# Performance work log

Measured on AMD Instinct MI355X. Metric: run time of the kernel, lower is better.

Reference implementation:

```python
import jax, jax.numpy as jnp
import numpy as np

B, S, D, H = 4, 2048, 1024, 16
DH = D // H  # 64


def setup_inputs() -> dict:
    key = jax.random.key(0)
    ks = jax.random.split(key, 11)
    s = 0.02
    return {
        "query": jax.random.normal(ks[0], (B, S, D), jnp.float32),
        "key": jax.random.normal(ks[1], (B, S, D), jnp.float32),
        "value": jax.random.normal(ks[2], (B, S, D), jnp.float32),
        "Wq": jax.random.normal(ks[3], (D, D), jnp.float32) * s,
        "bq": jnp.zeros((D,), jnp.float32),
        "Wk": jax.random.normal(ks[4], (D, D), jnp.float32) * s,
        "bk": jnp.zeros((D,), jnp.float32),
        "Wv": jax.random.normal(ks[5], (D, D), jnp.float32) * s,
        "bv": jnp.zeros((D,), jnp.float32),
        "Wo": jax.random.normal(ks[6], (D, D), jnp.float32) * s,
        "bo": jnp.zeros((D,), jnp.float32),
    }


def reference(query, key, value, Wq, bq, Wk, bk, Wv, bv, Wo, bo):
    b, s, _ = query.shape
    # linear projections (torch Linear: x @ W^T + b; here W stored as [in, out])
    q = query @ Wq + bq
    k = key @ Wk + bk
    v = value @ Wv + bv
    # split heads -> [B, H, S, DH]
    q = q.reshape(b, s, H, DH).transpose(0, 2, 1, 3)
    k = k.reshape(b, s, H, DH).transpose(0, 2, 1, 3)
    v = v.reshape(b, s, H, DH).transpose(0, 2, 1, 3)
    scale = jnp.sqrt(jnp.asarray(DH, jnp.float32))
    attn = jnp.einsum("bhqd,bhkd->bhqk", q, k) / scale  # [B,H,S,S]
    attn = jax.nn.softmax(attn, axis=-1)
    out = jnp.einsum("bhqk,bhkd->bhqd", attn, v)
    out = out.transpose(0, 2, 1, 3).reshape(b, s, D)
    return out @ Wo + bo
```

## Files before the change

kernel.cpp:

```cpp
#include <hip/hip_runtime.h>

typedef float f32x4 __attribute__((ext_vector_type(4)));
typedef __bf16 bf16x8 __attribute__((ext_vector_type(8)));
typedef unsigned short u16;
typedef unsigned int u32;
typedef u16 u16x4 __attribute__((ext_vector_type(4)));
typedef u16 u16x8 __attribute__((ext_vector_type(8)));
typedef u32 u32x2 __attribute__((ext_vector_type(2)));
typedef u32 u32x4 __attribute__((ext_vector_type(4)));

constexpr int Bn = 4, Sn = 2048, Dn = 1024, Hn = 16, DHn = 64;
constexpr int Mn = Bn * Sn;

static __device__ __forceinline__ u16 f2bf(float f) {
  return __builtin_bit_cast(u16, (__bf16)f);
}

static __device__ __forceinline__ u32 cvtpk(float lo, float hi) {
  u32 r;
  asm("v_cvt_pk_bf16_f32 %0, %1, %2" : "=v"(r) : "v"(lo), "v"(hi));
  return r;
}

static __device__ __forceinline__ void async16(const void* g, void* l) {
  __builtin_amdgcn_global_load_lds((const __attribute__((address_space(1))) u32*)g,
                                   (__attribute__((address_space(3))) u32*)l, 16, 0, 0);
}

static __device__ __forceinline__ void wait_bar2() {
  asm volatile("s_waitcnt vmcnt(2)" ::: "memory");
  __builtin_amdgcn_sched_barrier(0);
  __builtin_amdgcn_s_barrier();
  __builtin_amdgcn_sched_barrier(0);
}
static __device__ __forceinline__ void wait_bar8() {
  asm volatile("s_waitcnt vmcnt(8)" ::: "memory");
  __builtin_amdgcn_sched_barrier(0);
  __builtin_amdgcn_s_barrier();
  __builtin_amdgcn_sched_barrier(0);
}
static __device__ __forceinline__ void wait_bar0() {
  asm volatile("s_waitcnt vmcnt(0)" ::: "memory");
  __builtin_amdgcn_sched_barrier(0);
  __builtin_amdgcn_s_barrier();
  __builtin_amdgcn_sched_barrier(0);
}
static __device__ __forceinline__ void raw_bar() {
  __builtin_amdgcn_sched_barrier(0);
  __builtin_amdgcn_s_barrier();
  __builtin_amdgcn_sched_barrier(0);
}

__global__ void __launch_bounds__(256) cvt3_kernel(const float* __restrict__ q,
                                                   const float* __restrict__ k,
                                                   const float* __restrict__ v,
                                                   u16* __restrict__ dst) {
  const int i = blockIdx.x * 256 + threadIdx.x;
  const int t = i >> 20;
  const int li = i & 1048575;
  const float* s = (t == 0) ? q : (t == 1) ? k : v;
  const f32x4* sp = (const f32x4*)s + (size_t)li * 2;
  const f32x4 a = sp[0], b = sp[1];
  u16x8 o;
  o[0] = f2bf(a[0]); o[1] = f2bf(a[1]); o[2] = f2bf(a[2]); o[3] = f2bf(a[3]);
  o[4] = f2bf(b[0]); o[5] = f2bf(b[1]); o[6] = f2bf(b[2]); o[7] = f2bf(b[3]);
  ((u16x8*)dst)[i] = o;
}

__global__ void __launch_bounds__(256) transpose4_kernel(const float* __restrict__ Wq,
                                                         const float* __restrict__ Wk,
                                                         const float* __restrict__ Wv,
                                                         const float* __restrict__ Wo,
                                                         u16* __restrict__ Wts) {
  __shared__ float tile[32][33];
  const int z = blockIdx.z;
  const float* W = (z == 0) ? Wq : (z == 1) ? Wk : (z == 2) ? Wv : Wo;
  u16* Wt = Wts + (size_t)z * Dn * Dn;
  const int n0 = blockIdx.x * 32, k0 = blockIdx.y * 32;
  const int tx = threadIdx.x & 31, ty = (threadIdx.x >> 5) * 4;
#pragma unroll
  for (int i = 0; i < 4; ++i)
    tile[ty + i][tx] = W[(size_t)(k0 + ty + i) * Dn + n0 + tx];
  __syncthreads();
#pragma unroll
  for (int i = 0; i < 4; ++i)
    Wt[(size_t)(n0 + ty + i) * Dn + k0 + tx] = f2bf(tile[tx][ty + i]);
}

__global__ void __launch_bounds__(256) gemm_qkv_kernel(const u16* __restrict__ X,
                                                       const u16* __restrict__ Wts,
                                                       const float* __restrict__ bq,
                                                       const float* __restrict__ bk,
                                                       const float* __restrict__ bv,
                                                       u16* __restrict__ outbase) {
  __shared__ u16 As[2][128 * 64];
  __shared__ u16 Bs[2][128 * 64];

  const int bid = blockIdx.x;
  const int xcd = bid & 7;
  const int loc = bid >> 3;
  const int nb = loc & 7;
  const int panel = xcd * 24 + (loc >> 3);
  const int z = panel >> 6;
  const int m0 = (panel & 63) * 128, n0 = nb * 128;

  const u16* A = X + (size_t)z * Mn * Dn;
  const u16* Bt = Wts + (size_t)z * Dn * Dn;
  const float* bias = (z == 0) ? bq : (z == 1) ? bk : bv;
  u16* outp = outbase + (size_t)z * Mn * Dn;
  const float scale = (z == 0) ? 0.125f * 1.4426950408889634f : 1.0f;

  const int tid = threadIdx.x;
  const int wave = tid >> 6, lane = tid & 63;
  const int g = lane >> 4, c = lane & 15;
  const int wm = wave >> 1, wn = wave & 1;
  const int srow = lane >> 3, blk = lane & 7;

  f32x4 acc[4][4] = {};
  constexpr int NK = Dn / 64;

#pragma unroll
  for (int p = 0; p < 2; ++p) {
    const int k0 = p * 64;
#pragma unroll
    for (int i = 0; i < 4; ++i) {
      const int ch = wave * 4 + i;
      const int row = ch * 8 + srow;
      const int sblk = blk ^ srow;
      async16(A + (size_t)(m0 + row) * Dn + k0 + sblk * 8, As[p] + ch * 512);
      async16(Bt + (size_t)(n0 + row) * Dn + k0 + sblk * 8, Bs[p] + ch * 512);
    }
  }

  for (int k = 0; k < NK; ++k) {
    const int cur = k & 1;
    if (k + 1 < NK) wait_bar8(); else wait_bar0();

#pragma unroll
    for (int kk = 0; kk < 2; ++kk) {
      bf16x8 af[4], bfr[4];
#pragma unroll
      for (int mi = 0; mi < 4; ++mi)
        af[mi] = *(const bf16x8*)(As[cur] + (wm * 64 + mi * 16 + c) * 64 +
                                  (((kk * 4 + g) ^ (c & 7)) * 8));
#pragma unroll
      for (int ni = 0; ni < 4; ++ni)
        bfr[ni] = *(const bf16x8*)(Bs[cur] + (wn * 64 + ni * 16 + c) * 64 +
                                   (((kk * 4 + g) ^ (c & 7)) * 8));
#pragma unroll
      for (int mi = 0; mi < 4; ++mi)
#pragma unroll
        for (int ni = 0; ni < 4; ++ni)
          acc[mi][ni] = __builtin_amdgcn_mfma_f32_16x16x32_bf16(af[mi], bfr[ni],
                                                                acc[mi][ni], 0, 0, 0);
    }

    raw_bar();
    if (k + 2 < NK) {
      const int k0 = (k + 2) * 64;
#pragma unroll
      for (int i = 0; i < 4; ++i) {
        const int ch = wave * 4 + i;
        const int row = ch * 8 + srow;
        const int sblk = blk ^ srow;
        async16(A + (size_t)(m0 + row) * Dn + k0 + sblk * 8, As[cur] + ch * 512);
        async16(Bt + (size_t)(n0 + row) * Dn + k0 + sblk * 8, Bs[cur] + ch * 512);
      }
    }
  }

  const bool vmode = (z == 2);
#pragma unroll
  for (int ni = 0; ni < 4; ++ni) {
    const int col = n0 + wn * 64 + ni * 16 + c;
    const float bv = bias[col];
    const int hh = col >> 6, dh = col & 63;
#pragma unroll
    for (int mi = 0; mi < 4; ++mi) {
      const int row = m0 + wm * 64 + mi * 16 + g * 4;
      const int bb = row >> 11, s = row & 2047;
      if (!vmode) {
        u16* o = outp + (((size_t)(bb * Hn + hh) * Sn + s) * DHn + dh);
#pragma unroll
        for (int r = 0; r < 4; ++r)
          o[(size_t)r * DHn] = f2bf((acc[mi][ni][r] + bv) * scale);
      } else {
        u16x4 pk;
#pragma unroll
        for (int r = 0; r < 4; ++r) pk[r] = f2bf(acc[mi][ni][r] + bv);
        *(u16x4*)(outp + ((size_t)(bb * Hn + hh) * DHn + dh) * Sn + s) = pk;
      }
    }
  }
}

__global__ void __launch_bounds__(256) gemm_o_kernel(const u16* __restrict__ A,
                                                     const u16* __restrict__ Bt,
                                                     const float* __restrict__ bias,
                                                     float* __restrict__ outp) {
  __shared__ u16 As[2][128 * 64];
  __shared__ u16 Bs[2][128 * 64];
  const int bid = blockIdx.x;
  const int xcd = bid & 7;
  const int loc = bid >> 3;
  const int nb = loc & 7;
  const int panel = xcd * 8 + (loc >> 3);
  const int m0 = panel * 128, n0 = nb * 128;

  const int tid = threadIdx.x;
  const int wave = tid >> 6, lane = tid & 63;
  const int g = lane >> 4, c = lane & 15;
  const int wm = wave >> 1, wn = wave & 1;
  const int srow = lane >> 3, blk = lane & 7;

  f32x4 acc[4][4] = {};
  constexpr int NK = Dn / 64;

#pragma unroll
  for (int p = 0; p < 2; ++p) {
    const int k0 = p * 64;
#pragma unroll
    for (int i = 0; i < 4; ++i) {
      const int ch = wave * 4 + i;
      const int row = ch * 8 + srow;
      const int sblk = blk ^ srow;
      async16(A + (size_t)(m0 + row) * Dn + k0 + sblk * 8, As[p] + ch * 512);
      async16(Bt + (size_t)(n0 + row) * Dn + k0 + sblk * 8, Bs[p] + ch * 512);
    }
  }

  for (int k = 0; k < NK; ++k) {
    const int cur = k & 1;
    if (k + 1 < NK) wait_bar8(); else wait_bar0();

#pragma unroll
    for (int kk = 0; kk < 2; ++kk) {
      bf16x8 af[4], bfr[4];
#pragma unroll
      for (int mi = 0; mi < 4; ++mi)
        af[mi] = *(const bf16x8*)(As[cur] + (wm * 64 + mi * 16 + c) * 64 +
                                  (((kk * 4 + g) ^ (c & 7)) * 8));
#pragma unroll
      for (int ni = 0; ni < 4; ++ni)
        bfr[ni] = *(const bf16x8*)(Bs[cur] + (wn * 64 + ni * 16 + c) * 64 +
                                   (((kk * 4 + g) ^ (c & 7)) * 8));
#pragma unroll
      for (int mi = 0; mi < 4; ++mi)
#pragma unroll
        for (int ni = 0; ni < 4; ++ni)
          acc[mi][ni] = __builtin_amdgcn_mfma_f32_16x16x32_bf16(af[mi], bfr[ni],
                                                                acc[mi][ni], 0, 0, 0);
    }

    raw_bar();
    if (k + 2 < NK) {
      const int k0 = (k + 2) * 64;
#pragma unroll
      for (int i = 0; i < 4; ++i) {
        const int ch = wave * 4 + i;
        const int row = ch * 8 + srow;
        const int sblk = blk ^ srow;
        async16(A + (size_t)(m0 + row) * Dn + k0 + sblk * 8, As[cur] + ch * 512);
        async16(Bt + (size_t)(n0 + row) * Dn + k0 + sblk * 8, Bs[cur] + ch * 512);
      }
    }
  }

#pragma unroll
  for (int ni = 0; ni < 4; ++ni) {
    const int col = n0 + wn * 64 + ni * 16 + c;
    const float bv = bias[col];
#pragma unroll
    for (int mi = 0; mi < 4; ++mi) {
      const int row = m0 + wm * 64 + mi * 16 + g * 4;
      float* o = outp + (size_t)row * Dn + col;
#pragma unroll
      for (int r = 0; r < 4; ++r) o[(size_t)r * Dn] = acc[mi][ni][r] + bv;
    }
  }
}

__global__ void __launch_bounds__(512, 4) attn_kernel(const u16* __restrict__ Q,
                                                      const u16* __restrict__ Kp,
                                                      const u16* __restrict__ VT,
                                                      u16* __restrict__ O) {
  __shared__ u16 Ks[3][64 * 64];
  __shared__ u16 Vs[3][64 * 64];
  const int tid = threadIdx.x;
  const int wave = tid >> 6, lane = tid & 63;
  const int g = lane >> 4, c = lane & 15;
  const int bh = blockIdx.x;
  const int q0 = blockIdx.y * 256 + wave * 32;
  const u16* Qb = Q + (size_t)bh * Sn * DHn;
  const u16* Kb = Kp + (size_t)bh * Sn * DHn;
  const u16* Vb = VT + (size_t)bh * DHn * Sn;

  bf16x8 qf[2][2];
#pragma unroll
  for (int fq = 0; fq < 2; ++fq)
#pragma unroll
    for (int kk = 0; kk < 2; ++kk)
      qf[fq][kk] = *(const bf16x8*)(Qb + (size_t)(q0 + fq * 16 + c) * DHn + kk * 32 + g * 8);

  f32x4 ot[4][2] = {};
  f32x4 lacc[2] = {};
  u16x8 one8u;
#pragma unroll
  for (int j = 0; j < 8; ++j) one8u[j] = 0x3F80;
  const bf16x8 one8 = __builtin_bit_cast(bf16x8, one8u);
  const f32x4 zf = {};

  const int srow = lane >> 3, blk = lane & 7;
  const int krow = wave * 8 + srow;
  const int sblk = blk ^ srow;
  constexpr int NT = Sn / 64;

  u16 *kA = Ks[0], *kB = Ks[1], *kC = Ks[2];
  u16 *vA = Vs[0], *vB = Vs[1], *vC = Vs[2];

#pragma unroll
  for (int tt = 0; tt < 2; ++tt) {
    const int kt = tt * 64;
    async16(Kb + (size_t)(kt + krow) * DHn + sblk * 8, Ks[tt] + wave * 512);
    async16(Vb + (size_t)krow * Sn + kt + sblk * 8, Vs[tt] + wave * 512);
  }

  for (int t = 0; t < NT; ++t) {
    if (t + 1 < NT) wait_bar2(); else wait_bar0();

    if (t + 2 < NT) {
      const int kt = (t + 2) * 64;
      async16(Kb + (size_t)(kt + krow) * DHn + sblk * 8, kC + wave * 512);
      async16(Vb + (size_t)krow * Sn + kt + sblk * 8, vC + wave * 512);
    }

    f32x4 st[4][2];
    {
      bf16x8 kf[4];
#pragma unroll
      for (int fk = 0; fk < 4; ++fk)
        kf[fk] = *(const bf16x8*)(kA + (fk * 16 + c) * 64 + ((g ^ (c & 7)) * 8));
      __builtin_amdgcn_s_setprio(1);
#pragma unroll
      for (int fk = 0; fk < 4; ++fk)
#pragma unroll
        for (int fq = 0; fq < 2; ++fq)
          st[fk][fq] = __builtin_amdgcn_mfma_f32_16x16x32_bf16(kf[fk], qf[fq][0],
                                                               zf, 0, 0, 0);
      __builtin_amdgcn_s_setprio(0);
#pragma unroll
      for (int fk = 0; fk < 4; ++fk)
        kf[fk] = *(const bf16x8*)(kA + (fk * 16 + c) * 64 + (((4 + g) ^ (c & 7)) * 8));
      __builtin_amdgcn_s_setprio(1);
#pragma unroll
      for (int fk = 0; fk < 4; ++fk)
#pragma unroll
        for (int fq = 0; fq < 2; ++fq)
          st[fk][fq] = __builtin_amdgcn_mfma_f32_16x16x32_bf16(kf[fk], qf[fq][1],
                                                               st[fk][fq], 0, 0, 0);
      __builtin_amdgcn_s_setprio(0);
    }

#pragma unroll
    for (int fq = 0; fq < 2; ++fq)
#pragma unroll
      for (int fk = 0; fk < 4; ++fk)
#pragma unroll
        for (int r = 0; r < 4; ++r)
          st[fk][fq][r] = __builtin_amdgcn_exp2f(st[fk][fq][r]);

    bf16x8 pf[2][2];
#pragma unroll
    for (int fq = 0; fq < 2; ++fq)
#pragma unroll
      for (int kk = 0; kk < 2; ++kk) {
        u32x4 pw;
#pragma unroll
        for (int w = 0; w < 2; ++w) {
          const u32 a = cvtpk(st[2 * kk][fq][2 * w], st[2 * kk][fq][2 * w + 1]);
          const u32 b = cvtpk(st[2 * kk + 1][fq][2 * w], st[2 * kk + 1][fq][2 * w + 1]);
          const u32x2 p1 = __builtin_amdgcn_permlane32_swap(a, b, false, false);
          const u32x2 p2 = __builtin_amdgcn_permlane16_swap(p1[0], p1[1], false, false);
          pw[w] = p2[0];
          pw[2 + w] = p2[1];
        }
        pf[kk][fq] = __builtin_bit_cast(bf16x8, pw);
      }

#pragma unroll
    for (int kk = 0; kk < 2; ++kk) {
      bf16x8 vf[4];
#pragma unroll
      for (int fa = 0; fa < 4; ++fa)
        vf[fa] = *(const bf16x8*)(vA + (fa * 16 + c) * 64 +
                                  (((kk * 4 + g) ^ (c & 7)) * 8));
      __builtin_amdgcn_s_setprio(1);
#pragma unroll
      for (int fa = 0; fa < 4; ++fa)
#pragma unroll
        for (int fq = 0; fq < 2; ++fq)
          ot[fa][fq] = __builtin_amdgcn_mfma_f32_16x16x32_bf16(vf[fa], pf[kk][fq],
                                                               ot[fa][fq], 0, 0, 0);
#pragma unroll
      for (int fq = 0; fq < 2; ++fq)
        lacc[fq] = __builtin_amdgcn_mfma_f32_16x16x32_bf16(one8, pf[kk][fq],
                                                           lacc[fq], 0, 0, 0);
      __builtin_amdgcn_s_setprio(0);
    }

    u16* tk = kA; kA = kB; kB = kC; kC = tk;
    u16* tv = vA; vA = vB; vB = vC; vC = tv;
  }

  const int bb = bh >> 4, hh = bh & 15;
#pragma unroll
  for (int fq = 0; fq < 2; ++fq) {
    const float inv = 1.f / lacc[fq][0];
    const int s = q0 + fq * 16 + c;
#pragma unroll
    for (int fa = 0; fa < 4; ++fa) {
      const int dh = fa * 16 + g * 4;
      u16x4 pk;
#pragma unroll
      for (int r = 0; r < 4; ++r) pk[r] = f2bf(ot[fa][fq][r] * inv);
      *(u16x4*)(O + ((size_t)bb * Sn + s) * Dn + hh * 64 + dh) = pk;
    }
  }
}

extern "C" void kernel_launch(void* const* d_in, const int* in_sizes, int n_in,
                              void* d_out, int out_size, void* d_ws, size_t ws_size,
                              hipStream_t stream) {
  (void)in_sizes; (void)n_in; (void)out_size; (void)ws_size;
  const float* q_in = (const float*)d_in[0];
  const float* k_in = (const float*)d_in[1];
  const float* v_in = (const float*)d_in[2];
  const float* Wq = (const float*)d_in[3];
  const float* bq = (const float*)d_in[4];
  const float* Wk = (const float*)d_in[5];
  const float* bk = (const float*)d_in[6];
  const float* Wv = (const float*)d_in[7];
  const float* bv = (const float*)d_in[8];
  const float* Wo = (const float*)d_in[9];
  const float* bo = (const float*)d_in[10];

  char* ws = (char*)d_ws;
  const size_t szX = (size_t)Mn * Dn * 2;
  const size_t szW = (size_t)Dn * Dn * 2;
  u16* X = (u16*)ws;
  u16* Wts = (u16*)(ws + 3 * szX);
  u16* Qb = (u16*)(ws + 3 * szX + 4 * szW + 0 * szX);
  u16* Kb = (u16*)(ws + 3 * szX + 4 * szW + 1 * szX);
  u16* VTb = (u16*)(ws + 3 * szX + 4 * szW + 2 * szX);
  u16* Ob = (u16*)(ws + 3 * szX + 4 * szW + 3 * szX);

  cvt3_kernel<<<3 * Mn * Dn / 8 / 256, 256, 0, stream>>>(q_in, k_in, v_in, X);

  transpose4_kernel<<<dim3(32, 32, 4), 256, 0, stream>>>(Wq, Wk, Wv, Wo, Wts);

  gemm_qkv_kernel<<<1536, 256, 0, stream>>>(X, Wts, bq, bk, bv, Qb);

  attn_kernel<<<dim3(Bn * Hn, Sn / 256), 512, 0, stream>>>(Qb, Kb, VTb, Ob);

  gemm_o_kernel<<<512, 256, 0, stream>>>(Ob, Wts + (size_t)3 * Dn * Dn, bo,
                                         (float*)d_out);
}
```

Before: 181.9 us.

## Triple-buffer GEMM pipelines with 256x128 tiles and fuse prep kernels

```diff
diff --git a/kernel.cpp b/kernel.cpp
--- a/kernel.cpp
+++ b/kernel.cpp
@@ -33,8 +33,8 @@
   __builtin_amdgcn_s_barrier();
   __builtin_amdgcn_sched_barrier(0);
 }
-static __device__ __forceinline__ void wait_bar8() {
-  asm volatile("s_waitcnt vmcnt(8)" ::: "memory");
+static __device__ __forceinline__ void wait_bar6() {
+  asm volatile("s_waitcnt vmcnt(6)" ::: "memory");
   __builtin_amdgcn_sched_barrier(0);
   __builtin_amdgcn_s_barrier();
   __builtin_amdgcn_sched_barrier(0);
@@ -45,64 +45,63 @@
   __builtin_amdgcn_s_barrier();
   __builtin_amdgcn_sched_barrier(0);
 }
-static __device__ __forceinline__ void raw_bar() {
-  __builtin_amdgcn_sched_barrier(0);
-  __builtin_amdgcn_s_barrier();
-  __builtin_amdgcn_sched_barrier(0);
-}
-
-__global__ void __launch_bounds__(256) cvt3_kernel(const float* __restrict__ q,
+
+__global__ void __launch_bounds__(256) prep_kernel(const float* __restrict__ q,
                                                    const float* __restrict__ k,
                                                    const float* __restrict__ v,
-                                                   u16* __restrict__ dst) {
-  const int i = blockIdx.x * 256 + threadIdx.x;
-  const int t = i >> 20;
-  const int li = i & 1048575;
-  const float* s = (t == 0) ? q : (t == 1) ? k : v;
-  const f32x4* sp = (const f32x4*)s + (size_t)li * 2;
-  const f32x4 a = sp[0], b = sp[1];
-  u16x8 o;
-  o[0] = f2bf(a[0]); o[1] = f2bf(a[1]); o[2] = f2bf(a[2]); o[3] = f2bf(a[3]);
-  o[4] = f2bf(b[0]); o[5] = f2bf(b[1]); o[6] = f2bf(b[2]); o[7] = f2bf(b[3]);
-  ((u16x8*)dst)[i] = o;
-}
-
-__global__ void __launch_bounds__(256) transpose4_kernel(const float* __restrict__ Wq,
-                                                         const float* __restrict__ Wk,
-                                                         const float* __restrict__ Wv,
-                                                         const float* __restrict__ Wo,
-                                                         u16* __restrict__ Wts) {
+                                                   u16* __restrict__ X,
+                                                   const float* __restrict__ Wq,
+                                                   const float* __restrict__ Wk,
+                                                   const float* __restrict__ Wv,
+                                                   const float* __restrict__ Wo,
+                                                   u16* __restrict__ Wts) {
   __shared__ float tile[32][33];
-  const int z = blockIdx.z;
-  const float* W = (z == 0) ? Wq : (z == 1) ? Wk : (z == 2) ? Wv : Wo;
-  u16* Wt = Wts + (size_t)z * Dn * Dn;
-  const int n0 = blockIdx.x * 32, k0 = blockIdx.y * 32;
-  const int tx = threadIdx.x & 31, ty = (threadIdx.x >> 5) * 4;
-#pragma unroll
-  for (int i = 0; i < 4; ++i)
-    tile[ty + i][tx] = W[(size_t)(k0 + ty + i) * Dn + n0 + tx];
-  __syncthreads();
-#pragma unroll
-  for (int i = 0; i < 4; ++i)
-    Wt[(size_t)(n0 + ty + i) * Dn + k0 + tx] = f2bf(tile[tx][ty + i]);
-}
-
-__global__ void __launch_bounds__(256) gemm_qkv_kernel(const u16* __restrict__ X,
-                                                       const u16* __restrict__ Wts,
-                                                       const float* __restrict__ bq,
-                                                       const float* __restrict__ bk,
-                                                       const float* __restrict__ bv,
-                                                       u16* __restrict__ outbase) {
-  __shared__ u16 As[2][128 * 64];
-  __shared__ u16 Bs[2][128 * 64];
+  const int bid = blockIdx.x;
+  if (bid < 12288) {
+    const int i = bid * 256 + threadIdx.x;
+    const int t = i >> 20;
+    const int li = i & 1048575;
+    const float* s = (t == 0) ? q : (t == 1) ? k : v;
+    const f32x4* sp = (const f32x4*)s + (size_t)li * 2;
+    const f32x4 a = sp[0], b = sp[1];
+    u16x8 o;
+    o[0] = f2bf(a[0]); o[1] = f2bf(a[1]); o[2] = f2bf(a[2]); o[3] = f2bf(a[3]);
+    o[4] = f2bf(b[0]); o[5] = f2bf(b[1]); o[6] = f2bf(b[2]); o[7] = f2bf(b[3]);
+    ((u16x8*)X)[i] = o;
+  } else {
+    const int t = bid - 12288;
+    const int z = t >> 10;
+    const int rem = t & 1023;
+    const int n0 = (rem & 31) * 32, k0 = (rem >> 5) * 32;
+    const float* W = (z == 0) ? Wq : (z == 1) ? Wk : (z == 2) ? Wv : Wo;
+    u16* Wt = Wts + (size_t)z * Dn * Dn;
+    const int tx = threadIdx.x & 31, ty = (threadIdx.x >> 5) * 4;
+#pragma unroll
+    for (int i = 0; i < 4; ++i)
+      tile[ty + i][tx] = W[(size_t)(k0 + ty + i) * Dn + n0 + tx];
+    __syncthreads();
+#pragma unroll
+    for (int i = 0; i < 4; ++i)
+      Wt[(size_t)(n0 + ty + i) * Dn + k0 + tx] = f2bf(tile[tx][ty + i]);
+  }
+}
+
+__global__ void __launch_bounds__(512, 2) gemm_qkv_kernel(const u16* __restrict__ X,
+                                                          const u16* __restrict__ Wts,
+                                                          const float* __restrict__ bq,
+                                                          const float* __restrict__ bk,
+                                                          const float* __restrict__ bv,
+                                                          u16* __restrict__ outbase) {
+  __shared__ u16 As[3][256 * 64];
+  __shared__ u16 Bs[3][128 * 64];
 
   const int bid = blockIdx.x;
   const int xcd = bid & 7;
   const int loc = bid >> 3;
   const int nb = loc & 7;
-  const int panel = xcd * 24 + (loc >> 3);
-  const int z = panel >> 6;
-  const int m0 = (panel & 63) * 128, n0 = nb * 128;
+  const int panel = xcd * 12 + (loc >> 3);
+  const int z = panel >> 5;
+  const int m0 = (panel & 31) * 256, n0 = nb * 128;
 
   const u16* A = X + (size_t)z * Mn * Dn;
   const u16* Bt = Wts + (size_t)z * Dn * Dn;
@@ -115,58 +114,65 @@
   const int g = lane >> 4, c = lane & 15;
   const int wm = wave >> 1, wn = wave & 1;
   const int srow = lane >> 3, blk = lane & 7;
+  const int sblk = blk ^ srow;
 
   f32x4 acc[4][4] = {};
   constexpr int NK = Dn / 64;
 
-#pragma unroll
-  for (int p = 0; p < 2; ++p) {
-    const int k0 = p * 64;
+  auto stageA = [&](int k0, u16* dst) {
 #pragma unroll
     for (int i = 0; i < 4; ++i) {
-      const int ch = wave * 4 + i;
+      const int ch = i * 8 + wave;
       const int row = ch * 8 + srow;
-      const int sblk = blk ^ srow;
-      async16(A + (size_t)(m0 + row) * Dn + k0 + sblk * 8, As[p] + ch * 512);
-      async16(Bt + (size_t)(n0 + row) * Dn + k0 + sblk * 8, Bs[p] + ch * 512);
-    }
-  }
-
-  for (int k = 0; k < NK; ++k) {
-    const int cur = k & 1;
-    if (k + 1 < NK) wait_bar8(); else wait_bar0();
+      async16(A + (size_t)(m0 + row) * Dn + k0 + sblk * 8, dst + ch * 512);
+    }
+  };
+  auto stageB = [&](int k0, u16* dst) {
+#pragma unroll
+    for (int i = 0; i < 2; ++i) {
+      const int ch = i * 8 + wave;
+      const int row = ch * 8 + srow;
+      async16(Bt + (size_t)(n0 + row) * Dn + k0 + sblk * 8, dst + ch * 512);
+    }
+  };
+
+  u16 *aA = As[0], *aB = As[1], *aC = As[2];
+  u16 *bA = Bs[0], *bB = Bs[1], *bC = Bs[2];
+
+  stageA(0, aA);  stageB(0, bA);
+  stageA(64, aB); stageB(64, bB);
+
+  for (int t = 0; t < NK; ++t) {
+    if (t + 1 < NK) wait_bar6(); else wait_bar0();
+
+    if (t + 2 < NK) {
+      stageA((t + 2) * 64, aC);
+      stageB((t + 2) * 64, bC);
+    }
 
 #pragma unroll
     for (int kk = 0; kk < 2; ++kk) {
       bf16x8 af[4], bfr[4];
 #pragma unroll
       for (int mi = 0; mi < 4; ++mi)
-        af[mi] = *(const bf16x8*)(As[cur] + (wm * 64 + mi * 16 + c) * 64 +
+        af[mi] = *(const bf16x8*)(aA + (wm * 64 + mi * 16 + c) * 64 +
                                   (((kk * 4 + g) ^ (c & 7)) * 8));
 #pragma unroll
       for (int ni = 0; ni < 4; ++ni)
-        bfr[ni] = *(const bf16x8*)(Bs[cur] + (wn * 64 + ni * 16 + c) * 64 +
+        bfr[ni] = *(const bf16x8*)(bA + (wn * 64 + ni * 16 + c) * 64 +
                                    (((kk * 4 + g) ^ (c & 7)) * 8));
+      __builtin_amdgcn_s_setprio(1);
 #pragma unroll
       for (int mi = 0; mi < 4; ++mi)
 #pragma unroll
         for (int ni = 0; ni < 4; ++ni)
           acc[mi][ni] = __builtin_amdgcn_mfma_f32_16x16x32_bf16(af[mi], bfr[ni],
                                                                 acc[mi][ni], 0, 0, 0);
-    }
-
-    raw_bar();
-    if (k + 2 < NK) {
-      const int k0 = (k + 2) * 64;
-#pragma unroll
-      for (int i = 0; i < 4; ++i) {
-        const int ch = wave * 4 + i;
-        const int row = ch * 8 + srow;
-        const int sblk = blk ^ srow;
-        async16(A + (size_t)(m0 + row) * Dn + k0 + sblk * 8, As[cur] + ch * 512);
-        async16(Bt + (size_t)(n0 + row) * Dn + k0 + sblk * 8, Bs[cur] + ch * 512);
-      }
-    }
+      __builtin_amdgcn_s_setprio(0);
+    }
+
+    u16* ta = aA; aA = aB; aB = aC; aC = ta;
+    u16* tb = bA; bA = bB; bB = bC; bC = tb;
   }
 
   const bool vmode = (z == 2);
@@ -194,76 +200,84 @@
   }
 }
 
-__global__ void __launch_bounds__(256) gemm_o_kernel(const u16* __restrict__ A,
-                                                     const u16* __restrict__ Bt,
-                                                     const float* __restrict__ bias,
-                                                     float* __restrict__ outp) {
-  __shared__ u16 As[2][128 * 64];
-  __shared__ u16 Bs[2][128 * 64];
+__global__ void __launch_bounds__(512, 2) gemm_o_kernel(const u16* __restrict__ A,
+                                                        const u16* __restrict__ Bt,
+                                                        const float* __restrict__ bias,
+                                                        float* __restrict__ outp) {
+  __shared__ u16 As[3][256 * 64];
+  __shared__ u16 Bs[3][128 * 64];
+
   const int bid = blockIdx.x;
   const int xcd = bid & 7;
   const int loc = bid >> 3;
   const int nb = loc & 7;
-  const int panel = xcd * 8 + (loc >> 3);
-  const int m0 = panel * 128, n0 = nb * 128;
+  const int panel = xcd * 4 + (loc >> 3);
+  const int m0 = panel * 256, n0 = nb * 128;
 
   const int tid = threadIdx.x;
   const int wave = tid >> 6, lane = tid & 63;
   const int g = lane >> 4, c = lane & 15;
   const int wm = wave >> 1, wn = wave & 1;
   const int srow = lane >> 3, blk = lane & 7;
+  const int sblk = blk ^ srow;
 
   f32x4 acc[4][4] = {};
   constexpr int NK = Dn / 64;
 
-#pragma unroll
-  for (int p = 0; p < 2; ++p) {
-    const int k0 = p * 64;
+  auto stageA = [&](int k0, u16* dst) {
 #pragma unroll
     for (int i = 0; i < 4; ++i) {
-      const int ch = wave * 4 + i;
+      const int ch = i * 8 + wave;
       const int row = ch * 8 + srow;
-      const int sblk = blk ^ srow;
-      async16(A + (size_t)(m0 + row) * Dn + k0 + sblk * 8, As[p] + ch * 512);
-      async16(Bt + (size_t)(n0 + row) * Dn + k0 + sblk * 8, Bs[p] + ch * 512);
-    }
-  }
-
-  for (int k = 0; k < NK; ++k) {
-    const int cur = k & 1;
-    if (k + 1 < NK) wait_bar8(); else wait_bar0();
+      async16(A + (size_t)(m0 + row) * Dn + k0 + sblk * 8, dst + ch * 512);
+    }
+  };
+  auto stageB = [&](int k0, u16* dst) {
+#pragma unroll
+    for (int i = 0; i < 2; ++i) {
+      const int ch = i * 8 + wave;
+      const int row = ch * 8 + srow;
+      async16(Bt + (size_t)(n0 + row) * Dn + k0 + sblk * 8, dst + ch * 512);
+    }
+  };
+
+  u16 *aA = As[0], *aB = As[1], *aC = As[2];
+  u16 *bA = Bs[0], *bB = Bs[1], *bC = Bs[2];
+
+  stageA(0, aA);  stageB(0, bA);
+  stageA(64, aB); stageB(64, bB);
+
+  for (int t = 0; t < NK; ++t) {
+    if (t + 1 < NK) wait_bar6(); else wait_bar0();
+
+    if (t + 2 < NK) {
+      stageA((t + 2) * 64, aC);
+      stageB((t + 2) * 64, bC);
+    }
 
 #pragma unroll
     for (int kk = 0; kk < 2; ++kk) {
       bf16x8 af[4], bfr[4];
 #pragma unroll
       for (int mi = 0; mi < 4; ++mi)
-        af[mi] = *(const bf16x8*)(As[cur] + (wm * 64 + mi * 16 + c) * 64 +
+        af[mi] = *(const bf16x8*)(aA + (wm * 64 + mi * 16 + c) * 64 +
                                   (((kk * 4 + g) ^ (c & 7)) * 8));
 #pragma unroll
       for (int ni = 0; ni < 4; ++ni)
-        bfr[ni] = *(const bf16x8*)(Bs[cur] + (wn * 64 + ni * 16 + c) * 64 +
+        bfr[ni] = *(const bf16x8*)(bA + (wn * 64 + ni * 16 + c) * 64 +
                                    (((kk * 4 + g) ^ (c & 7)) * 8));
+      __builtin_amdgcn_s_setprio(1);
 #pragma unroll
       for (int mi = 0; mi < 4; ++mi)
 #pragma unroll
         for (int ni = 0; ni < 4; ++ni)
           acc[mi][ni] = __builtin_amdgcn_mfma_f32_16x16x32_bf16(af[mi], bfr[ni],
                                                                 acc[mi][ni], 0, 0, 0);
-    }
-
-    raw_bar();
-    if (k + 2 < NK) {
-      const int k0 = (k + 2) * 64;
-#pragma unroll
-      for (int i = 0; i < 4; ++i) {
-        const int ch = wave * 4 + i;
-        const int row = ch * 8 + srow;
-        const int sblk = blk ^ srow;
-        async16(A + (size_t)(m0 + row) * Dn + k0 + sblk * 8, As[cur] + ch * 512);
-        async16(Bt + (size_t)(n0 + row) * Dn + k0 + sblk * 8, Bs[cur] + ch * 512);
-      }
-    }
+      __builtin_amdgcn_s_setprio(0);
+    }
+
+    u16* ta = aA; aA = aB; aB = aC; aC = ta;
+    u16* tb = bA; bA = bB; bB = bC; bC = tb;
   }
 
 #pragma unroll
@@ -454,14 +468,12 @@
   u16* VTb = (u16*)(ws + 3 * szX + 4 * szW + 2 * szX);
   u16* Ob = (u16*)(ws + 3 * szX + 4 * szW + 3 * szX);
 
-  cvt3_kernel<<<3 * Mn * Dn / 8 / 256, 256, 0, stream>>>(q_in, k_in, v_in, X);
-
-  transpose4_kernel<<<dim3(32, 32, 4), 256, 0, stream>>>(Wq, Wk, Wv, Wo, Wts);
-
-  gemm_qkv_kernel<<<1536, 256, 0, stream>>>(X, Wts, bq, bk, bv, Qb);
+  prep_kernel<<<16384, 256, 0, stream>>>(q_in, k_in, v_in, X, Wq, Wk, Wv, Wo, Wts);
+
+  gemm_qkv_kernel<<<768, 512, 0, stream>>>(X, Wts, bq, bk, bv, Qb);
 
   attn_kernel<<<dim3(Bn * Hn, Sn / 256), 512, 0, stream>>>(Qb, Kb, VTb, Ob);
 
-  gemm_o_kernel<<<512, 256, 0, stream>>>(Ob, Wts + (size_t)3 * Dn * Dn, bo,
+  gemm_o_kernel<<<256, 512, 0, stream>>>(Ob, Wts + (size_t)3 * Dn * Dn, bo,
                                          (float*)d_out);
 }
```

After: 194.5 us. +7.0%, slower.

## Triple-buffer QKV GEMM with K=32 tiles and merge prep kernels

Applied to the files above, without the earlier changes.

```diff
diff --git a/kernel.cpp b/kernel.cpp
--- a/kernel.cpp
+++ b/kernel.cpp
@@ -33,6 +33,12 @@
   __builtin_amdgcn_s_barrier();
   __builtin_amdgcn_sched_barrier(0);
 }
+static __device__ __forceinline__ void wait_bar4() {
+  asm volatile("s_waitcnt vmcnt(4)" ::: "memory");
+  __builtin_amdgcn_sched_barrier(0);
+  __builtin_amdgcn_s_barrier();
+  __builtin_amdgcn_sched_barrier(0);
+}
 static __device__ __forceinline__ void wait_bar8() {
   asm volatile("s_waitcnt vmcnt(8)" ::: "memory");
   __builtin_amdgcn_sched_barrier(0);
@@ -51,40 +57,44 @@
   __builtin_amdgcn_sched_barrier(0);
 }
 
-__global__ void __launch_bounds__(256) cvt3_kernel(const float* __restrict__ q,
+__global__ void __launch_bounds__(256) prep_kernel(const float* __restrict__ q,
                                                    const float* __restrict__ k,
                                                    const float* __restrict__ v,
-                                                   u16* __restrict__ dst) {
-  const int i = blockIdx.x * 256 + threadIdx.x;
-  const int t = i >> 20;
-  const int li = i & 1048575;
-  const float* s = (t == 0) ? q : (t == 1) ? k : v;
-  const f32x4* sp = (const f32x4*)s + (size_t)li * 2;
-  const f32x4 a = sp[0], b = sp[1];
-  u16x8 o;
-  o[0] = f2bf(a[0]); o[1] = f2bf(a[1]); o[2] = f2bf(a[2]); o[3] = f2bf(a[3]);
-  o[4] = f2bf(b[0]); o[5] = f2bf(b[1]); o[6] = f2bf(b[2]); o[7] = f2bf(b[3]);
-  ((u16x8*)dst)[i] = o;
-}
-
-__global__ void __launch_bounds__(256) transpose4_kernel(const float* __restrict__ Wq,
-                                                         const float* __restrict__ Wk,
-                                                         const float* __restrict__ Wv,
-                                                         const float* __restrict__ Wo,
-                                                         u16* __restrict__ Wts) {
+                                                   u16* __restrict__ X,
+                                                   const float* __restrict__ Wq,
+                                                   const float* __restrict__ Wk,
+                                                   const float* __restrict__ Wv,
+                                                   const float* __restrict__ Wo,
+                                                   u16* __restrict__ Wts) {
   __shared__ float tile[32][33];
-  const int z = blockIdx.z;
-  const float* W = (z == 0) ? Wq : (z == 1) ? Wk : (z == 2) ? Wv : Wo;
-  u16* Wt = Wts + (size_t)z * Dn * Dn;
-  const int n0 = blockIdx.x * 32, k0 = blockIdx.y * 32;
-  const int tx = threadIdx.x & 31, ty = (threadIdx.x >> 5) * 4;
-#pragma unroll
-  for (int i = 0; i < 4; ++i)
-    tile[ty + i][tx] = W[(size_t)(k0 + ty + i) * Dn + n0 + tx];
-  __syncthreads();
-#pragma unroll
-  for (int i = 0; i < 4; ++i)
-    Wt[(size_t)(n0 + ty + i) * Dn + k0 + tx] = f2bf(tile[tx][ty + i]);
+  const int bid = blockIdx.x;
+  if (bid < 12288) {
+    const int i = bid * 256 + threadIdx.x;
+    const int t = i >> 20;
+    const int li = i & 1048575;
+    const float* s = (t == 0) ? q : (t == 1) ? k : v;
+    const f32x4* sp = (const f32x4*)s + (size_t)li * 2;
+    const f32x4 a = sp[0], b = sp[1];
+    u16x8 o;
+    o[0] = f2bf(a[0]); o[1] = f2bf(a[1]); o[2] = f2bf(a[2]); o[3] = f2bf(a[3]);
+    o[4] = f2bf(b[0]); o[5] = f2bf(b[1]); o[6] = f2bf(b[2]); o[7] = f2bf(b[3]);
+    ((u16x8*)X)[i] = o;
+  } else {
+    const int t = bid - 12288;
+    const int z = t >> 10;
+    const int rem = t & 1023;
+    const int n0 = (rem & 31) * 32, k0 = (rem >> 5) * 32;
+    const float* W = (z == 0) ? Wq : (z == 1) ? Wk : (z == 2) ? Wv : Wo;
+    u16* Wt = Wts + (size_t)z * Dn * Dn;
+    const int tx = threadIdx.x & 31, ty = (threadIdx.x >> 5) * 4;
+#pragma unroll
+    for (int i = 0; i < 4; ++i)
+      tile[ty + i][tx] = W[(size_t)(k0 + ty + i) * Dn + n0 + tx];
+    __syncthreads();
+#pragma unroll
+    for (int i = 0; i < 4; ++i)
+      Wt[(size_t)(n0 + ty + i) * Dn + k0 + tx] = f2bf(tile[tx][ty + i]);
+  }
 }
 
 __global__ void __launch_bounds__(256) gemm_qkv_kernel(const u16* __restrict__ X,
@@ -93,8 +103,8 @@
                                                        const float* __restrict__ bk,
                                                        const float* __restrict__ bv,
                                                        u16* __restrict__ outbase) {
-  __shared__ u16 As[2][128 * 64];
-  __shared__ u16 Bs[2][128 * 64];
+  __shared__ u16 As[3][128 * 32];
+  __shared__ u16 Bs[3][128 * 32];
 
   const int bid = blockIdx.x;
   const int xcd = bid & 7;
@@ -104,8 +114,8 @@
   const int z = panel >> 6;
   const int m0 = (panel & 63) * 128, n0 = nb * 128;
 
-  const u16* A = X + (size_t)z * Mn * Dn;
-  const u16* Bt = Wts + (size_t)z * Dn * Dn;
+  const u16* A = X + (size_t)z * Mn * Dn + (size_t)m0 * Dn;
+  const u16* Bt = Wts + (size_t)z * Dn * Dn + (size_t)n0 * Dn;
   const float* bias = (z == 0) ? bq : (z == 1) ? bk : bv;
   u16* outp = outbase + (size_t)z * Mn * Dn;
   const float scale = (z == 0) ? 0.125f * 1.4426950408889634f : 1.0f;
@@ -114,59 +124,58 @@
   const int wave = tid >> 6, lane = tid & 63;
   const int g = lane >> 4, c = lane & 15;
   const int wm = wave >> 1, wn = wave & 1;
-  const int srow = lane >> 3, blk = lane & 7;
 
   f32x4 acc[4][4] = {};
-  constexpr int NK = Dn / 64;
-
-#pragma unroll
-  for (int p = 0; p < 2; ++p) {
-    const int k0 = p * 64;
-#pragma unroll
-    for (int i = 0; i < 4; ++i) {
-      const int ch = wave * 4 + i;
-      const int row = ch * 8 + srow;
-      const int sblk = blk ^ srow;
-      async16(A + (size_t)(m0 + row) * Dn + k0 + sblk * 8, As[p] + ch * 512);
-      async16(Bt + (size_t)(n0 + row) * Dn + k0 + sblk * 8, Bs[p] + ch * 512);
-    }
-  }
-
-  for (int k = 0; k < NK; ++k) {
-    const int cur = k & 1;
-    if (k + 1 < NK) wait_bar8(); else wait_bar0();
-
-#pragma unroll
-    for (int kk = 0; kk < 2; ++kk) {
-      bf16x8 af[4], bfr[4];
-#pragma unroll
-      for (int mi = 0; mi < 4; ++mi)
-        af[mi] = *(const bf16x8*)(As[cur] + (wm * 64 + mi * 16 + c) * 64 +
-                                  (((kk * 4 + g) ^ (c & 7)) * 8));
+  constexpr int NT = Dn / 32;
+
+  auto stage = [&](const u16* src, int k0, u16* dst) {
+#pragma unroll
+    for (int i = 0; i < 2; ++i) {
+      const int ch = wave * 2 + i;
+      const int line = ch * 8 + (lane >> 3);
+      const int s8 = (lane & 7) ^ (line & 7);
+      const int grow = 2 * line + (s8 >> 2);
+      async16(src + (size_t)grow * Dn + k0 + (s8 & 3) * 8, dst + ch * 512);
+    }
+  };
+  auto lds_off = [](int r, int gg) {
+    const int line = r >> 1;
+    const int q = (r & 1) * 4 + gg;
+    return line * 64 + ((q ^ (line & 7)) * 8);
+  };
+
+  u16 *aA = As[0], *aB = As[1], *aC = As[2];
+  u16 *bA = Bs[0], *bB = Bs[1], *bC = Bs[2];
+
+  stage(A, 0, aA);  stage(Bt, 0, bA);
+  stage(A, 32, aB); stage(Bt, 32, bB);
+
+  for (int t = 0; t < NT; ++t) {
+    if (t + 1 < NT) wait_bar4(); else wait_bar0();
+
+    if (t + 2 < NT) {
+      stage(A, (t + 2) * 32, aC);
+      stage(Bt, (t + 2) * 32, bC);
+    }
+
+    bf16x8 af[4], bfr[4];
+#pragma unroll
+    for (int mi = 0; mi < 4; ++mi)
+      af[mi] = *(const bf16x8*)(aA + lds_off(wm * 64 + mi * 16 + c, g));
+#pragma unroll
+    for (int ni = 0; ni < 4; ++ni)
+      bfr[ni] = *(const bf16x8*)(bA + lds_off(wn * 64 + ni * 16 + c, g));
+    __builtin_amdgcn_s_setprio(1);
+#pragma unroll
+    for (int mi = 0; mi < 4; ++mi)
 #pragma unroll
       for (int ni = 0; ni < 4; ++ni)
-        bfr[ni] = *(const bf16x8*)(Bs[cur] + (wn * 64 + ni * 16 + c) * 64 +
-                                   (((kk * 4 + g) ^ (c & 7)) * 8));
-#pragma unroll
-      for (int mi = 0; mi < 4; ++mi)
-#pragma unroll
-        for (int ni = 0; ni < 4; ++ni)
-          acc[mi][ni] = __builtin_amdgcn_mfma_f32_16x16x32_bf16(af[mi], bfr[ni],
-                                                                acc[mi][ni], 0, 0, 0);
-    }
-
-    raw_bar();
-    if (k + 2 < NK) {
-      const int k0 = (k + 2) * 64;
-#pragma unroll
-      for (int i = 0; i < 4; ++i) {
-        const int ch = wave * 4 + i;
-        const int row = ch * 8 + srow;
-        const int sblk = blk ^ srow;
-        async16(A + (size_t)(m0 + row) * Dn + k0 + sblk * 8, As[cur] + ch * 512);
-        async16(Bt + (size_t)(n0 + row) * Dn + k0 + sblk * 8, Bs[cur] + ch * 512);
-      }
-    }
+        acc[mi][ni] = __builtin_amdgcn_mfma_f32_16x16x32_bf16(af[mi], bfr[ni],
+                                                              acc[mi][ni], 0, 0, 0);
+    __builtin_amdgcn_s_setprio(0);
+
+    u16* ta = aA; aA = aB; aB = aC; aC = ta;
+    u16* tb = bA; bA = bB; bB = bC; bC = tb;
   }
 
   const bool vmode = (z == 2);
@@ -454,9 +463,7 @@
   u16* VTb = (u16*)(ws + 3 * szX + 4 * szW + 2 * szX);
   u16* Ob = (u16*)(ws + 3 * szX + 4 * szW + 3 * szX);
 
-  cvt3_kernel<<<3 * Mn * Dn / 8 / 256, 256, 0, stream>>>(q_in, k_in, v_in, X);
-
-  transpose4_kernel<<<dim3(32, 32, 4), 256, 0, stream>>>(Wq, Wk, Wv, Wo, Wts);
+  prep_kernel<<<16384, 256, 0, stream>>>(q_in, k_in, v_in, X, Wq, Wk, Wv, Wo, Wts);
 
   gemm_qkv_kernel<<<1536, 256, 0, stream>>>(X, Wts, bq, bk, bv, Qb);
 
```

Result: no change. 185.1 us (+1.8%).
